# Performance work log

Measured on AMD Instinct MI355X. Metric: run time of the kernel, lower is better.

Reference implementation:

```python
import jax, jax.numpy as jnp
import numpy as np

NUM_EXPERTS = 64
TOP_K = 2
TEMPERATURE = 1.0
MOMENTUM = 0.9


def _l2norm(x, axis=-1):
    # torch F.normalize: x / max(||x||, eps)
    n = jnp.linalg.norm(x, axis=axis, keepdims=True)
    return x / jnp.maximum(n, 1e-12)


def setup_inputs() -> dict:
    key = jax.random.key(0)
    k1, k2 = jax.random.split(key)
    hidden_states = jax.random.normal(k1, (4, 4096, 2048), dtype=jnp.float32)
    centers = _l2norm(jax.random.normal(k2, (NUM_EXPERTS, 2048), dtype=jnp.float32))
    return {"hidden_states": hidden_states, "centers": centers}


def reference(hidden_states, centers):
    B, T, H = hidden_states.shape
    flat = hidden_states.reshape(-1, H).astype(jnp.float32)  # [N, H]
    N = flat.shape[0]

    # cosine-similarity logits
    reps_n = _l2norm(flat)
    centers_n = _l2norm(centers)
    temp = jnp.maximum(jnp.float32(TEMPERATURE), 1e-6)
    logits = (reps_n @ centers_n.T) / temp  # [N, E]

    probs = jax.nn.softmax(logits, axis=-1)
    top_w, top_ids = jax.lax.top_k(probs, TOP_K)  # [N, k]
    top_w = top_w / (jnp.sum(top_w, axis=-1, keepdims=True) + 1e-9)

    # EMA center update from top-1 routed expert (training+update path)
    route = top_ids[:, 0]  # [N]
    sums = jax.ops.segment_sum(flat, route, num_segments=NUM_EXPERTS)  # [E, H]
    counts = jax.ops.segment_sum(jnp.ones((N, 1), jnp.float32), route,
                                 num_segments=NUM_EXPERTS)  # [E, 1]
    means = sums / (counts + 1e-6)
    updated = _l2norm(MOMENTUM * centers + (1.0 - MOMENTUM) * means)
    new_centers = jnp.where(counts > 0, updated, centers)

    top_ids = top_ids.reshape(B, T, TOP_K)
    top_w = top_w.reshape(B, T, TOP_K)
    return top_ids, top_w, new_centers
```

## Files before the change

### kernel.cpp

```cpp
#include <hip/hip_runtime.h>
#include <math.h>

#define NTOK 16384
#define HDIM 2048
#define NEXP 64
#define KK   32
#define TAU  5e-5f
#define MAXB 2048
#define KP2  40
#define LTS2 68

typedef __attribute__((ext_vector_type(8))) short short8;
typedef __attribute__((ext_vector_type(4))) float f32x4;
typedef __attribute__((ext_vector_type(2))) unsigned int uint2v;


__global__ __launch_bounds__(256)
void zero_kernel(float* p, int n) {
  int i = blockIdx.x * 256 + threadIdx.x;
  if (i < n) p[i] = 0.0f;
}

__device__ __forceinline__ float block_reduce_sum(float v, float* red) {
  #pragma unroll
  for (int o = 32; o > 0; o >>= 1) v += __shfl_down(v, o, 64);
  int lane = threadIdx.x & 63;
  int wid  = threadIdx.x >> 6;
  if (lane == 0) red[wid] = v;
  __syncthreads();
  float s = red[0] + red[1] + red[2] + red[3];
  __syncthreads();
  return s;
}

__device__ __forceinline__ double block_reduce_sum_f64(double v, double* red) {
  const int tid = threadIdx.x;
  red[tid] = v;
  __syncthreads();
  if (tid < 128) red[tid] += red[tid + 128];
  __syncthreads();
  if (tid < 64)  red[tid] += red[tid + 64];
  __syncthreads();
  double s = 0.0;
  if (tid < 64) {
    s = red[tid];
    #pragma unroll
    for (int o = 32; o > 0; o >>= 1) s += __shfl_down(s, o, 64);
  }
  if (tid == 0) red[0] = s;
  __syncthreads();
  s = red[0];
  __syncthreads();
  return s;
}

__global__ __launch_bounds__(256)
void cnorm_kernel(const float* __restrict__ c, float* __restrict__ inv_nc) {
  __shared__ float red[4];
  int e = blockIdx.x;
  float ss = 0.f;
  #pragma unroll
  for (int j = 0; j < 8; ++j) {
    float v = c[e * HDIM + threadIdx.x + j * 256];
    ss += v * v;
  }
  float tot = block_reduce_sum(ss, red);
  if (threadIdx.x == 0) inv_nc[e] = 1.0f / fmaxf(sqrtf(tot), 1e-12f);
}

__global__ __launch_bounds__(256)
void cprep_kernel(const float* __restrict__ c, float* __restrict__ inv_nc,
                  float* __restrict__ bn, unsigned short* __restrict__ cbh,
                  unsigned short* __restrict__ cbl, int* __restrict__ zr,
                  int* __restrict__ cnt) {
  __shared__ float red[4];
  __shared__ double redd[256];
  __shared__ float s_nc;
  const int e = blockIdx.x;
  const int tid = threadIdx.x;
  if (e == 0 && tid < 128) zr[tid] = 0;
  if (e == 1 && tid < 64)  cnt[tid] = 0;
  const float* cr = c + (size_t)e * HDIM;
  float ss = 0.f;
  double acc = 0.0;
  #pragma unroll
  for (int j = 0; j < 8; ++j) {
    float v = cr[tid + j * 256];
    ss += v * v;
    double dv = (double)v;
    acc += dv * dv;
  }
  float tot = block_reduce_sum(ss, red);
  double cn = block_reduce_sum_f64(acc, redd);
  if (tid == 0) {
    inv_nc[e] = 1.0f / fmaxf(sqrtf(tot), 1e-12f);
    s_nc = (float)fmax(sqrt(cn), 1e-12);
  }
  __syncthreads();
  const double nc = (double)s_nc;
  #pragma unroll
  for (int j = 0; j < 8; ++j) {
    const int k = tid + j * 256;
    const float v = cr[k];
    bn[(size_t)e * HDIM + k] = (float)((double)v / nc);
    unsigned u = __float_as_uint(v);
    unsigned h = u & 0xffff0000u;
    float r = v - __uint_as_float(h);
    cbh[(size_t)e * HDIM + k] = (unsigned short)(u >> 16);
    cbl[(size_t)e * HDIM + k] = (unsigned short)(__float_as_uint(r) >> 16);
  }
}

__device__ __forceinline__ void cvt2(float v0, float v1, unsigned &hi, unsigned &lo) {
  unsigned u0 = __float_as_uint(v0);
  unsigned u1 = __float_as_uint(v1);
  unsigned h0 = u0 & 0xffff0000u;
  unsigned h1 = u1 & 0xffff0000u;
  float r0 = v0 - __uint_as_float(h0);
  float r1 = v1 - __uint_as_float(h1);
  hi = (u0 >> 16) | h1;
  lo = (__float_as_uint(r0) >> 16) | (__float_as_uint(r1) & 0xffff0000u);
}

__global__ __launch_bounds__(256)
void gemm_part(const float* __restrict__ x,
               const unsigned short* __restrict__ cbh,
               const unsigned short* __restrict__ cbl,
               float* __restrict__ lp, float* __restrict__ xnp) {
  __shared__ __align__(16) unsigned short smem[10240];
  unsigned short (*Ah)[KP2] = (unsigned short (*)[KP2])(smem);
  unsigned short (*Al)[KP2] = (unsigned short (*)[KP2])(smem + 2560);
  unsigned short (*Bh)[KP2] = (unsigned short (*)[KP2])(smem + 5120);
  unsigned short (*Bl)[KP2] = (unsigned short (*)[KP2])(smem + 7680);

  const int tid  = threadIdx.x;
  const int mt   = blockIdx.x >> 3;
  const int ks   = blockIdx.x & 7;
  const int t0   = mt * 64;
  const int kb   = ks * 256;
  const int sr   = tid >> 2;
  const int sq   = (tid & 3) * 8;
  const int lane = tid & 63;
  const int w    = tid >> 6;
  const int tw   = (w & 1) * 32;
  const int ew   = (w >> 1) * 32;
  const int fr   = lane & 15;
  const int fk   = (lane >> 4) * 8;

  const float*          xrow  = x   + (size_t)(t0 + sr) * HDIM + kb + sq;
  const unsigned short* bhrow = cbh + (size_t)sr * HDIM + kb + sq;
  const unsigned short* blrow = cbl + (size_t)sr * HDIM + kb + sq;

  f32x4 xp0, xp1;
  short8 bhp, blp;
  float nacc = 0.f;

  xp0 = *(const f32x4*)(xrow);
  xp1 = *(const f32x4*)(xrow + 4);
  bhp = *(const short8*)(bhrow);
  blp = *(const short8*)(blrow);

  f32x4 acc[2][2];
  #pragma unroll
  for (int mi = 0; mi < 2; ++mi)
    #pragma unroll
    for (int ni = 0; ni < 2; ++ni)
      acc[mi][ni] = (f32x4){0.f, 0.f, 0.f, 0.f};

  for (int it = 0; it < 8; ++it) {
    __syncthreads();
    {
      unsigned h01, l01, h23, l23, h45, l45, h67, l67;
      cvt2(xp0.x, xp0.y, h01, l01);
      cvt2(xp0.z, xp0.w, h23, l23);
      cvt2(xp1.x, xp1.y, h45, l45);
      cvt2(xp1.z, xp1.w, h67, l67);
      *(uint2v*)&Ah[sr][sq]     = (uint2v){h01, h23};
      *(uint2v*)&Ah[sr][sq + 4] = (uint2v){h45, h67};
      *(uint2v*)&Al[sr][sq]     = (uint2v){l01, l23};
      *(uint2v*)&Al[sr][sq + 4] = (uint2v){l45, l67};
      nacc += xp0.x*xp0.x + xp0.y*xp0.y + xp0.z*xp0.z + xp0.w*xp0.w
            + xp1.x*xp1.x + xp1.y*xp1.y + xp1.z*xp1.z + xp1.w*xp1.w;
      *(short8*)&Bh[sr][sq] = bhp;
      *(short8*)&Bl[sr][sq] = blp;
    }
    __syncthreads();
    if (it < 7) {
      const int o = (it + 1) * KK;
      xp0 = *(const f32x4*)(xrow + o);
      xp1 = *(const f32x4*)(xrow + o + 4);
      bhp = *(const short8*)(bhrow + o);
      blp = *(const short8*)(blrow + o);
    }
    short8 ah0 = *(const short8*)&Ah[tw + fr][fk];
    short8 ah1 = *(const short8*)&Ah[tw + 16 + fr][fk];
    short8 al0 = *(const short8*)&Al[tw + fr][fk];
    short8 al1 = *(const short8*)&Al[tw + 16 + fr][fk];
    #pragma unroll
    for (int ni = 0; ni < 2; ++ni) {
      short8 bh = *(const short8*)&Bh[ew + ni * 16 + fr][fk];
      short8 bl = *(const short8*)&Bl[ew + ni * 16 + fr][fk];
      acc[0][ni] = __builtin_amdgcn_mfma_f32_16x16x32_bf16(ah0, bh, acc[0][ni], 0, 0, 0);
      acc[0][ni] = __builtin_amdgcn_mfma_f32_16x16x32_bf16(ah0, bl, acc[0][ni], 0, 0, 0);
      acc[0][ni] = __builtin_amdgcn_mfma_f32_16x16x32_bf16(al0, bh, acc[0][ni], 0, 0, 0);
      acc[1][ni] = __builtin_amdgcn_mfma_f32_16x16x32_bf16(ah1, bh, acc[1][ni], 0, 0, 0);
      acc[1][ni] = __builtin_amdgcn_mfma_f32_16x16x32_bf16(ah1, bl, acc[1][ni], 0, 0, 0);
      acc[1][ni] = __builtin_amdgcn_mfma_f32_16x16x32_bf16(al1, bh, acc[1][ni], 0, 0, 0);
    }
  }

  float s = nacc;
  s += __shfl_xor(s, 1, 64);
  s += __shfl_xor(s, 2, 64);
  if ((tid & 3) == 0) xnp[ks * NTOK + t0 + sr] = s;

  __syncthreads();
  float* lt = (float*)smem;
  const int tloc = tw + (lane >> 4) * 4;
  #pragma unroll
  for (int mi = 0; mi < 2; ++mi)
    #pragma unroll
    for (int ni = 0; ni < 2; ++ni)
      *(f32x4*)&lt[(ew + ni * 16 + fr) * LTS2 + tloc + mi * 16] = acc[mi][ni];
  __syncthreads();
  #pragma unroll
  for (int n = 0; n < 16; ++n) {
    const int f = tid + n * 256;
    const int e = f >> 6;
    const int t = f & 63;
    lp[(size_t)(ks * NEXP + e) * NTOK + t0 + t] = lt[e * LTS2 + t];
  }
}

__global__ __launch_bounds__(512)
void softmax2_kernel(const float* __restrict__ lp, const float* __restrict__ xnp,
                     const float* __restrict__ inv_nc, float* __restrict__ out,
                     int* __restrict__ route, int* __restrict__ nflag,
                     int* __restrict__ flags, int* __restrict__ cursor,
                     int* __restrict__ cnt, int* __restrict__ bucket,
                     int* __restrict__ posa) {
  __shared__ float lg[NEXP][68];
  __shared__ float snc[NEXP];
  const int tid  = threadIdx.x;
  const int lane = tid & 63;
  const int w    = tid >> 6;
  const int kg   = w >> 2;
  const int eg   = (w & 3) * 16;
  const int t0   = blockIdx.x * 64;
  const int t    = t0 + lane;
  if (tid < NEXP) snc[tid] = inv_nc[tid];

  float p[16];
  const float* base = lp + (size_t)(kg * 4 * NEXP + eg) * NTOK + t;
  #pragma unroll
  for (int e = 0; e < 16; ++e) {
    const float* q = base + (size_t)e * NTOK;
    float a0 = q[0];
    float a1 = q[(size_t)NEXP * NTOK];
    float a2 = q[(size_t)2 * NEXP * NTOK];
    float a3 = q[(size_t)3 * NEXP * NTOK];
    p[e] = (a0 + a1) + (a2 + a3);
  }
  if (kg == 0) {
    #pragma unroll
    for (int e = 0; e < 16; ++e) lg[eg + e][lane] = p[e];
  }
  __syncthreads();
  if (kg == 1) {
    #pragma unroll
    for (int e = 0; e < 16; ++e) lg[eg + e][lane] += p[e];
  }
  __syncthreads();

  if (tid < 64) {
    float xs2 = 0.f;
    #pragma unroll
    for (int k = 0; k < 8; ++k) xs2 += xnp[k * NTOK + t];
    const float inv_nx = 1.0f / fmaxf(sqrtf(xs2), 1e-12f);
    float m1 = -1e30f, m2 = -1e30f, m3 = -1e30f;
    int i1 = 0, i2 = 0;
    #pragma unroll
    for (int e = 0; e < NEXP; ++e) {
      float l = lg[e][lane] * snc[e] * inv_nx;
      if (l > m1)      { m3 = m2; m2 = m1; i2 = i1; m1 = l; i1 = e; }
      else if (l > m2) { m3 = m2; m2 = l; i2 = e; }
      else if (l > m3) { m3 = l; }
    }
    float Z = 0.f;
    #pragma unroll
    for (int e = 0; e < NEXP; ++e)
      Z += expf(lg[e][lane] * snc[e] * inv_nx - m1);
    const float p1w = 1.0f / Z;
    const float p2w = expf(m2 - m1) / Z;
    const float s2  = p1w + p2w + 1e-9f;
    out[t * 2 + 0] = (float)i1;
    out[t * 2 + 1] = (float)i2;
    out[2 * NTOK + t * 2 + 0] = p1w / s2;
    out[2 * NTOK + t * 2 + 1] = p2w / s2;
    route[t] = i1;
    const int p0 = atomicAdd(&cursor[i1], 1);
    atomicAdd(&cnt[i1], 1);
    if (p0 < MAXB) bucket[i1 * MAXB + p0] = t;
    posa[t] = p0;
    if ((m1 - m2) < TAU || (m2 - m3) < TAU) {
      int idx = atomicAdd(nflag, 1);
      flags[idx] = t;
    }
  }
}

__global__ __launch_bounds__(256)
void refine_np_kernel(const float* __restrict__ x, const float* __restrict__ bn,
                      float* __restrict__ out, int* __restrict__ route,
                      const int* __restrict__ nflag, const int* __restrict__ flags,
                      int* __restrict__ cursor, int* __restrict__ cnt,
                      int* __restrict__ bucket, int* __restrict__ posa) {
  __shared__ float a_lds[HDIM];
  __shared__ double redd[256];
  __shared__ float lf[NEXP];
  __shared__ float s_nx;
  const int tid  = threadIdx.x;
  const int lane = tid & 63;
  const int w    = tid >> 6;
  const int n = *nflag;
  for (int j = blockIdx.x; j < n; j += gridDim.x) {
    const int t = flags[j];
    const float* xr = x + (size_t)t * HDIM;
    double xacc = 0.0;
    #pragma unroll
    for (int i = 0; i < 8; ++i) {
      double v = (double)xr[tid + 256 * i];
      xacc += v * v;
    }
    double xn = block_reduce_sum_f64(xacc, redd);
    if (tid == 0) s_nx = (float)fmax(sqrt(xn), 1e-12);
    __syncthreads();
    const double nx = (double)s_nx;
    #pragma unroll
    for (int i = 0; i < 8; ++i) {
      int k = tid + 256 * i;
      a_lds[k] = (float)((double)xr[k] / nx);
    }
    __syncthreads();
    #pragma unroll 1
    for (int ei = 0; ei < 16; ++ei) {
      const int e = w * 16 + ei;
      const float* br = bn + (size_t)e * HDIM;
      double d = 0.0;
      #pragma unroll 8
      for (int i = 0; i < 32; ++i) {
        int k = lane + 64 * i;
        d += (double)a_lds[k] * (double)br[k];
      }
      #pragma unroll
      for (int o = 32; o > 0; o >>= 1) d += __shfl_down(d, o, 64);
      if (lane == 0) lf[e] = (float)d;
    }
    __syncthreads();
    if (tid == 0) {
      float m32 = lf[0];
      for (int ee = 1; ee < NEXP; ++ee) m32 = fmaxf(m32, lf[ee]);
      float ex[NEXP];
      for (int ee = 0; ee < NEXP; ++ee)
        ex[ee] = (float)exp((double)(lf[ee] - m32));
      float r[8];
      #pragma unroll
      for (int q = 0; q < 8; ++q) r[q] = ex[q];
      for (int i = 8; i < NEXP; i += 8)
        #pragma unroll
        for (int q = 0; q < 8; ++q) r[q] += ex[i + q];
      const float Z = ((r[0] + r[1]) + (r[2] + r[3])) + ((r[4] + r[5]) + (r[6] + r[7]));
      float p1 = -1.f, p2 = -1.f;
      int i1 = 0, i2 = 0;
      for (int ee = 0; ee < NEXP; ++ee) {
        float p = ex[ee] / Z;
        if (p > p1)      { p2 = p1; i2 = i1; p1 = p; i1 = ee; }
        else if (p > p2) { p2 = p; i2 = ee; }
      }
      const float s = (p1 + p2) + 1e-9f;
      out[t * 2 + 0] = (float)i1;
      out[t * 2 + 1] = (float)i2;
      out[2 * NTOK + t * 2 + 0] = p1 / s;
      out[2 * NTOK + t * 2 + 1] = p2 / s;
      const int old = route[t];
      if (i1 != old) {
        const int p_old = posa[t];
        if (p_old < MAXB) bucket[old * MAXB + p_old] = -1;
        atomicSub(&cnt[old], 1);
        const int p = atomicAdd(&cursor[i1], 1);
        atomicAdd(&cnt[i1], 1);
        if (p < MAXB) bucket[i1 * MAXB + p] = t;
        posa[t] = p;
        route[t] = i1;
      }
    }
    __syncthreads();
  }
}

__global__ __launch_bounds__(64)
void refine_np_slow(const float* __restrict__ x, const float* __restrict__ c,
                    float* __restrict__ out, int* __restrict__ route,
                    const int* __restrict__ nflag, const int* __restrict__ flags) {
  __shared__ float lf[NEXP];
  const int e = threadIdx.x;
  const int n = *nflag;
  for (int j = blockIdx.x; j < n; j += gridDim.x) {
    const int t = flags[j];
    const float* xr = x + (size_t)t * HDIM;
    const float* cr = c + (size_t)e * HDIM;
    double xn = 0.0, cn = 0.0;
    for (int k = 0; k < HDIM; ++k) {
      double xv = (double)xr[k];
      double cv = (double)cr[k];
      xn += xv * xv;
      cn += cv * cv;
    }
    const float nx32 = (float)fmax(sqrt(xn), 1e-12);
    const float nc32 = (float)fmax(sqrt(cn), 1e-12);
    double d = 0.0;
    for (int k = 0; k < HDIM; ++k) {
      float a = (float)((double)xr[k] / (double)nx32);
      float b = (float)((double)cr[k] / (double)nc32);
      d += (double)a * (double)b;
    }
    lf[e] = (float)d;
    __syncthreads();
    if (e == 0) {
      float m32 = lf[0];
      for (int ee = 1; ee < NEXP; ++ee) m32 = fmaxf(m32, lf[ee]);
      float ex[NEXP];
      for (int ee = 0; ee < NEXP; ++ee)
        ex[ee] = (float)exp((double)(lf[ee] - m32));
      float r[8];
      #pragma unroll
      for (int q = 0; q < 8; ++q) r[q] = ex[q];
      for (int i = 8; i < NEXP; i += 8)
        #pragma unroll
        for (int q = 0; q < 8; ++q) r[q] += ex[i + q];
      const float Z = ((r[0] + r[1]) + (r[2] + r[3])) + ((r[4] + r[5]) + (r[6] + r[7]));
      float p1 = -1.f, p2 = -1.f;
      int i1 = 0, i2 = 0;
      for (int ee = 0; ee < NEXP; ++ee) {
        float p = ex[ee] / Z;
        if (p > p1)      { p2 = p1; i2 = i1; p1 = p; i1 = ee; }
        else if (p > p2) { p2 = p; i2 = ee; }
      }
      const float s = (p1 + p2) + 1e-9f;
      out[t * 2 + 0] = (float)i1;
      out[t * 2 + 1] = (float)i2;
      out[2 * NTOK + t * 2 + 0] = p1 / s;
      out[2 * NTOK + t * 2 + 1] = p2 / s;
      route[t] = i1;
    }
    __syncthreads();
  }
}

__global__ __launch_bounds__(256)
void segsum_part(const float* __restrict__ x, const int* __restrict__ cursor,
                 const int* __restrict__ bucket, float* __restrict__ psum) {
  __shared__ f32x4 part[4][64];
  const int e   = blockIdx.x >> 5;
  const int hc  = (blockIdx.x >> 2) & 7;
  const int ts  = blockIdx.x & 3;
  const int hb  = hc * 256;
  const int tid = threadIdx.x;
  const int rg  = tid >> 6;
  const int cc  = tid & 63;
  int n = cursor[e];
  if (n > MAXB) n = MAXB;
  const int nq = (n + 3) >> 2;
  const int lo = ts * nq;
  const int hi = min(lo + nq, n);
  const int* bk = bucket + e * MAXB;
  f32x4 a = (f32x4){0.f, 0.f, 0.f, 0.f};
  #pragma unroll 4
  for (int i = lo + rg; i < hi; i += 4) {
    const int r = bk[i];
    if (r >= 0) a += *(const f32x4*)(x + (size_t)r * HDIM + hb + cc * 4);
  }
  part[rg][cc] = a;
  __syncthreads();
  if (tid < 64) {
    f32x4 s = part[0][tid] + part[1][tid] + part[2][tid] + part[3][tid];
    *(f32x4*)&psum[(size_t)(ts * NEXP + e) * HDIM + hb + tid * 4] = s;
  }
}

__global__ __launch_bounds__(256)
void finalize4_kernel(const float* __restrict__ c, const float* __restrict__ psum,
                      const int* __restrict__ counts, float* __restrict__ out) {
  __shared__ float red[4];
  const int e = blockIdx.x;
  const int tid = threadIdx.x;
  const float cnt = (float)counts[e];
  const float minv = 1.0f / (cnt + 1e-6f);
  float u[8], cv[8];
  float ss = 0.f;
  #pragma unroll
  for (int j = 0; j < 8; ++j) {
    int h = tid + j * 256;
    cv[j] = c[e * HDIM + h];
    float sm = psum[(size_t)(0 * NEXP + e) * HDIM + h]
             + psum[(size_t)(1 * NEXP + e) * HDIM + h]
             + psum[(size_t)(2 * NEXP + e) * HDIM + h]
             + psum[(size_t)(3 * NEXP + e) * HDIM + h];
    float mean = sm * minv;
    u[j] = 0.9f * cv[j] + 0.1f * mean;
    ss += u[j] * u[j];
  }
  float tot = block_reduce_sum(ss, red);
  float sc = 1.0f / fmaxf(sqrtf(tot), 1e-12f);
  const bool nz = cnt > 0.f;
  #pragma unroll
  for (int j = 0; j < 8; ++j) {
    int h = tid + j * 256;
    out[4 * NTOK + e * HDIM + h] = nz ? u[j] * sc : cv[j];
  }
}

__global__ __launch_bounds__(256)
void finalize_kernel(const float* __restrict__ c, const float* __restrict__ sums,
                     const int* __restrict__ counts, float* __restrict__ out) {
  __shared__ float red[4];
  const int e = blockIdx.x;
  const int tid = threadIdx.x;
  const float cnt = (float)counts[e];
  const float minv = 1.0f / (cnt + 1e-6f);
  float u[8], cv[8];
  float ss = 0.f;
  #pragma unroll
  for (int j = 0; j < 8; ++j) {
    int h = tid + j * 256;
    cv[j] = c[e * HDIM + h];
    float mean = sums[e * HDIM + h] * minv;
    u[j] = 0.9f * cv[j] + 0.1f * mean;
    ss += u[j] * u[j];
  }
  float tot = block_reduce_sum(ss, red);
  float sc = 1.0f / fmaxf(sqrtf(tot), 1e-12f);
  const bool nz = cnt > 0.f;
  #pragma unroll
  for (int j = 0; j < 8; ++j) {
    int h = tid + j * 256;
    out[4 * NTOK + e * HDIM + h] = nz ? u[j] * sc : cv[j];
  }
}

__global__ __launch_bounds__(256)
void router_kernel(const float* __restrict__ x, const float* __restrict__ c,
                   const float* __restrict__ inv_nc, float* __restrict__ out,
                   int* __restrict__ route, int* __restrict__ nflag,
                   int* __restrict__ flags) {
  __shared__ __align__(16) float xs[64][36];
  __shared__ float lgs[64][67];
  const int tid  = threadIdx.x;
  const int lane = tid & 63;
  const int w    = tid >> 6;
  const int t0   = blockIdx.x * 64;
  const int e0   = __builtin_amdgcn_readfirstlane(w * 16);
  const float* cb = c + (size_t)e0 * HDIM;
  const int st = tid >> 3;
  const int sk = (tid & 7) * 4;
  float acc[16];
  #pragma unroll
  for (int e = 0; e < 16; ++e) acc[e] = 0.f;
  float nacc = 0.f;
  float4 p0 = *(const float4*)&x[(size_t)(t0 + st)      * HDIM + sk];
  float4 p1 = *(const float4*)&x[(size_t)(t0 + st + 32) * HDIM + sk];
  for (int k0 = 0; k0 < HDIM; k0 += 32) {
    __syncthreads();
    *(float4*)&xs[st][sk]      = p0;
    *(float4*)&xs[st + 32][sk] = p1;
    __syncthreads();
    const int kn = k0 + 32;
    if (kn < HDIM) {
      p0 = *(const float4*)&x[(size_t)(t0 + st)      * HDIM + kn + sk];
      p1 = *(const float4*)&x[(size_t)(t0 + st + 32) * HDIM + kn + sk];
    }
    float a[32];
    #pragma unroll
    for (int j = 0; j < 32; j += 4) {
      float4 v = *(const float4*)&xs[lane][j];
      a[j] = v.x; a[j+1] = v.y; a[j+2] = v.z; a[j+3] = v.w;
    }
    if (w == 0) {
      #pragma unroll
      for (int j = 0; j < 32; ++j) nacc += a[j] * a[j];
    }
    #pragma unroll
    for (int e = 0; e < 16; ++e) {
      const float* br = cb + (size_t)e * HDIM + k0;
      #pragma unroll
      for (int j = 0; j < 32; j += 4) {
        float4 bv = *(const float4*)&br[j];
        acc[e] += a[j]*bv.x + a[j+1]*bv.y + a[j+2]*bv.z + a[j+3]*bv.w;
      }
    }
  }
  #pragma unroll
  for (int e = 0; e < 16; ++e) lgs[lane][e0 + e] = acc[e] * inv_nc[e0 + e];
  __syncthreads();
  if (w == 0) {
    const float inv_nx = 1.0f / fmaxf(sqrtf(nacc), 1e-12f);
    float m1 = -1e30f, m2 = -1e30f, m3 = -1e30f;
    int i1 = 0, i2 = 0;
    for (int e = 0; e < NEXP; ++e) {
      float l = lgs[lane][e] * inv_nx;
      if (l > m1)      { m3 = m2; m2 = m1; i2 = i1; m1 = l; i1 = e; }
      else if (l > m2) { m3 = m2; m2 = l; i2 = e; }
      else if (l > m3) { m3 = l; }
    }
    float Z = 0.f;
    for (int e = 0; e < NEXP; ++e) Z += expf(lgs[lane][e] * inv_nx - m1);
    const float p1w = 1.0f / Z;
    const float p2w = expf(m2 - m1) / Z;
    const float s   = p1w + p2w + 1e-9f;
    const int tg = t0 + lane;
    out[tg * 2 + 0] = (float)i1;
    out[tg * 2 + 1] = (float)i2;
    out[2 * NTOK + tg * 2 + 0] = p1w / s;
    out[2 * NTOK + tg * 2 + 1] = p2w / s;
    route[tg] = i1;
    if ((m1 - m2) < TAU || (m2 - m3) < TAU) {
      int idx = atomicAdd(nflag, 1);
      flags[idx] = tg;
    }
  }
}

__global__ __launch_bounds__(512)
void segsum_kernel(const float* __restrict__ x, const int* __restrict__ route,
                   float* __restrict__ sums, int* __restrict__ counts) {
  __shared__ float ls[NEXP * 256];
  __shared__ int lcnt[NEXP];
  const int tid  = threadIdx.x;
  const int lane = tid & 63;
  const int w    = tid >> 6;
  const int hc   = blockIdx.x & 7;
  const int tg   = blockIdx.x >> 3;
  const int hb   = hc * 256;
  #pragma unroll
  for (int i = 0; i < 32; ++i) ls[tid + i * 512] = 0.f;
  if (tid < NEXP) lcnt[tid] = 0;
  __syncthreads();
  const int tbase = tg * 512 + w * 64;
  #pragma unroll 4
  for (int i = 0; i < 64; ++i) {
    const int t = tbase + i;
    const int e = route[t];
    const float* xr = x + (size_t)t * HDIM + hb + lane;
    #pragma unroll
    for (int j = 0; j < 4; ++j)
      atomicAdd(&ls[e * 256 + lane + 64 * j], xr[64 * j]);
    if (hc == 0 && lane == 0) atomicAdd(&lcnt[e], 1);
  }
  __syncthreads();
  #pragma unroll
  for (int i = tid; i < NEXP * 256; i += 512) {
    const int e = i >> 8, h = i & 255;
    atomicAdd(&sums[e * HDIM + hb + h], ls[i]);
  }
  if (hc == 0 && tid < NEXP && lcnt[tid] > 0) atomicAdd(&counts[tid], lcnt[tid]);
}

extern "C" void kernel_launch(void* const* d_in, const int* in_sizes, int n_in,
                              void* d_out, int out_size, void* d_ws, size_t ws_size,
                              hipStream_t stream) {
  const float* x = (const float*)d_in[0];
  const float* c = (const float*)d_in[1];
  float* out = (float*)d_out;
  float* ws = (float*)d_ws;

  float* inv_nc = ws;
  int*   cursor = (int*)(ws + 64);
  int*   nflag  = (int*)(ws + 128);
  int*   route  = (int*)(ws + 192);
  int*   flags  = (int*)(ws + 16576);
  float* sums   = ws + 32960;
  float* bn     = ws + 164032;
  unsigned short* cbh = (unsigned short*)(ws + 295104);
  unsigned short* cbl = (unsigned short*)(ws + 360640);
  int*   bucket = (int*)(ws + 426176);
  float* psum   = ws + 557248;
  int*   posa   = (int*)(ws + 1081536);
  int*   cnt    = (int*)(ws + 1097920);
  float* lp     = ws + 1097984;
  float* xnp    = ws + 9486592;

  const size_t NEED = 9617664ull * 4ull;
  if (ws_size >= NEED) {
    cprep_kernel<<<NEXP, 256, 0, stream>>>(c, inv_nc, bn, cbh, cbl, cursor, cnt);
    gemm_part<<<2048, 256, 0, stream>>>(x, cbh, cbl, lp, xnp);
    softmax2_kernel<<<NTOK / 64, 512, 0, stream>>>(lp, xnp, inv_nc, out, route,
                                                   nflag, flags, cursor, cnt, bucket, posa);
    refine_np_kernel<<<512, 256, 0, stream>>>(x, bn, out, route, nflag, flags,
                                              cursor, cnt, bucket, posa);
    segsum_part<<<2048, 256, 0, stream>>>(x, cursor, bucket, psum);
    finalize4_kernel<<<NEXP, 256, 0, stream>>>(c, psum, cnt, out);
  } else {
    zero_kernel<<<1, 256, 0, stream>>>(ws + 64, 128);
    zero_kernel<<<512, 256, 0, stream>>>(sums, 131072);
    cnorm_kernel<<<NEXP, 256, 0, stream>>>(c, inv_nc);
    router_kernel<<<NTOK / 64, 256, 0, stream>>>(x, c, inv_nc, out, route, nflag, flags);
    refine_np_slow<<<1024, 64, 0, stream>>>(x, c, out, route, nflag, flags);
    segsum_kernel<<<256, 512, 0, stream>>>(x, route, sums, cursor);
    finalize_kernel<<<NEXP, 256, 0, stream>>>(c, sums, cursor, out);
  }
}
```

Before: 312.2 us.

## Double-buffer GEMM register prefetch and parallelize softmax top-k across wave lanes

The logits GEMM kernel now prefetches global tiles into two alternating register sets, so the load for step it+2 is issued while step it is computed. The softmax kernel stops using 64 threads for the whole top-2 and softmax work. Each wave now handles 8 tokens, with one expert per lane, and finds top-3 values and the softmax denominator by cross-lane shuffle reductions. This spreads the serial 64-expert scan over all 512 threads, at the cost of many shuffles per token. It also changes the LDS padding, which may cause bank conflicts on the transposed lg reads.

```diff
diff --git a/kernel.cpp b/kernel.cpp
--- a/kernel.cpp
+++ b/kernel.cpp
@@ -151,14 +151,9 @@
   const unsigned short* bhrow = cbh + (size_t)sr * HDIM + kb + sq;
   const unsigned short* blrow = cbl + (size_t)sr * HDIM + kb + sq;
 
-  f32x4 xp0, xp1;
-  short8 bhp, blp;
   float nacc = 0.f;
-
-  xp0 = *(const f32x4*)(xrow);
-  xp1 = *(const f32x4*)(xrow + 4);
-  bhp = *(const short8*)(bhrow);
-  blp = *(const short8*)(blrow);
+  f32x4 Ax0, Ax1, Bx0, Bx1;
+  short8 Abh, Abl, Bbh, Bbl;
 
   f32x4 acc[2][2];
   #pragma unroll
@@ -167,47 +162,63 @@
     for (int ni = 0; ni < 2; ++ni)
       acc[mi][ni] = (f32x4){0.f, 0.f, 0.f, 0.f};
 
-  for (int it = 0; it < 8; ++it) {
-    __syncthreads();
-    {
-      unsigned h01, l01, h23, l23, h45, l45, h67, l67;
-      cvt2(xp0.x, xp0.y, h01, l01);
-      cvt2(xp0.z, xp0.w, h23, l23);
-      cvt2(xp1.x, xp1.y, h45, l45);
-      cvt2(xp1.z, xp1.w, h67, l67);
-      *(uint2v*)&Ah[sr][sq]     = (uint2v){h01, h23};
-      *(uint2v*)&Ah[sr][sq + 4] = (uint2v){h45, h67};
-      *(uint2v*)&Al[sr][sq]     = (uint2v){l01, l23};
-      *(uint2v*)&Al[sr][sq + 4] = (uint2v){l45, l67};
-      nacc += xp0.x*xp0.x + xp0.y*xp0.y + xp0.z*xp0.z + xp0.w*xp0.w
-            + xp1.x*xp1.x + xp1.y*xp1.y + xp1.z*xp1.z + xp1.w*xp1.w;
-      *(short8*)&Bh[sr][sq] = bhp;
-      *(short8*)&Bl[sr][sq] = blp;
-    }
-    __syncthreads();
-    if (it < 7) {
-      const int o = (it + 1) * KK;
-      xp0 = *(const f32x4*)(xrow + o);
-      xp1 = *(const f32x4*)(xrow + o + 4);
-      bhp = *(const short8*)(bhrow + o);
-      blp = *(const short8*)(blrow + o);
-    }
-    short8 ah0 = *(const short8*)&Ah[tw + fr][fk];
-    short8 ah1 = *(const short8*)&Ah[tw + 16 + fr][fk];
-    short8 al0 = *(const short8*)&Al[tw + fr][fk];
-    short8 al1 = *(const short8*)&Al[tw + 16 + fr][fk];
-    #pragma unroll
-    for (int ni = 0; ni < 2; ++ni) {
-      short8 bh = *(const short8*)&Bh[ew + ni * 16 + fr][fk];
-      short8 bl = *(const short8*)&Bl[ew + ni * 16 + fr][fk];
-      acc[0][ni] = __builtin_amdgcn_mfma_f32_16x16x32_bf16(ah0, bh, acc[0][ni], 0, 0, 0);
-      acc[0][ni] = __builtin_amdgcn_mfma_f32_16x16x32_bf16(ah0, bl, acc[0][ni], 0, 0, 0);
-      acc[0][ni] = __builtin_amdgcn_mfma_f32_16x16x32_bf16(al0, bh, acc[0][ni], 0, 0, 0);
-      acc[1][ni] = __builtin_amdgcn_mfma_f32_16x16x32_bf16(ah1, bh, acc[1][ni], 0, 0, 0);
-      acc[1][ni] = __builtin_amdgcn_mfma_f32_16x16x32_bf16(ah1, bl, acc[1][ni], 0, 0, 0);
-      acc[1][ni] = __builtin_amdgcn_mfma_f32_16x16x32_bf16(al1, bh, acc[1][ni], 0, 0, 0);
-    }
-  }
+  #define LDREG(P, it_) do { const int o_ = (it_) * KK;                   \
+    P##x0 = *(const f32x4*)(xrow + o_);                                   \
+    P##x1 = *(const f32x4*)(xrow + o_ + 4);                               \
+    P##bh = *(const short8*)(bhrow + o_);                                 \
+    P##bl = *(const short8*)(blrow + o_); } while (0)
+
+  #define STAGE(P) do {                                                   \
+    unsigned h01, l01, h23, l23, h45, l45, h67, l67;                      \
+    cvt2(P##x0.x, P##x0.y, h01, l01);                                     \
+    cvt2(P##x0.z, P##x0.w, h23, l23);                                     \
+    cvt2(P##x1.x, P##x1.y, h45, l45);                                     \
+    cvt2(P##x1.z, P##x1.w, h67, l67);                                     \
+    *(uint2v*)&Ah[sr][sq]     = (uint2v){h01, h23};                       \
+    *(uint2v*)&Ah[sr][sq + 4] = (uint2v){h45, h67};                       \
+    *(uint2v*)&Al[sr][sq]     = (uint2v){l01, l23};                       \
+    *(uint2v*)&Al[sr][sq + 4] = (uint2v){l45, l67};                       \
+    nacc += P##x0.x*P##x0.x + P##x0.y*P##x0.y + P##x0.z*P##x0.z + P##x0.w*P##x0.w \
+          + P##x1.x*P##x1.x + P##x1.y*P##x1.y + P##x1.z*P##x1.z + P##x1.w*P##x1.w; \
+    *(short8*)&Bh[sr][sq] = P##bh;                                        \
+    *(short8*)&Bl[sr][sq] = P##bl; } while (0)
+
+  #define MFMAS() do {                                                    \
+    short8 ah0 = *(const short8*)&Ah[tw + fr][fk];                        \
+    short8 ah1 = *(const short8*)&Ah[tw + 16 + fr][fk];                   \
+    short8 al0 = *(const short8*)&Al[tw + fr][fk];                        \
+    short8 al1 = *(const short8*)&Al[tw + 16 + fr][fk];                   \
+    _Pragma("unroll")                                                     \
+    for (int ni = 0; ni < 2; ++ni) {                                      \
+      short8 bh = *(const short8*)&Bh[ew + ni * 16 + fr][fk];             \
+      short8 bl = *(const short8*)&Bl[ew + ni * 16 + fr][fk];             \
+      acc[0][ni] = __builtin_amdgcn_mfma_f32_16x16x32_bf16(ah0, bh, acc[0][ni], 0, 0, 0); \
+      acc[0][ni] = __builtin_amdgcn_mfma_f32_16x16x32_bf16(ah0, bl, acc[0][ni], 0, 0, 0); \
+      acc[0][ni] = __builtin_amdgcn_mfma_f32_16x16x32_bf16(al0, bh, acc[0][ni], 0, 0, 0); \
+      acc[1][ni] = __builtin_amdgcn_mfma_f32_16x16x32_bf16(ah1, bh, acc[1][ni], 0, 0, 0); \
+      acc[1][ni] = __builtin_amdgcn_mfma_f32_16x16x32_bf16(ah1, bl, acc[1][ni], 0, 0, 0); \
+      acc[1][ni] = __builtin_amdgcn_mfma_f32_16x16x32_bf16(al1, bh, acc[1][ni], 0, 0, 0); \
+    } } while (0)
+
+  LDREG(A, 0);
+  LDREG(B, 1);
+
+  #pragma unroll 1
+  for (int it = 0; it < 8; it += 2) {
+    __syncthreads();
+    STAGE(A);
+    __syncthreads();
+    if (it + 2 < 8) LDREG(A, it + 2);
+    MFMAS();
+    __syncthreads();
+    STAGE(B);
+    __syncthreads();
+    if (it + 3 < 8) LDREG(B, it + 3);
+    MFMAS();
+  }
+  #undef LDREG
+  #undef STAGE
+  #undef MFMAS
 
   float s = nacc;
   s += __shfl_xor(s, 1, 64);
@@ -239,7 +250,8 @@
                      int* __restrict__ flags, int* __restrict__ cursor,
                      int* __restrict__ cnt, int* __restrict__ bucket,
                      int* __restrict__ posa) {
-  __shared__ float lg[NEXP][68];
+  __shared__ float lg[NEXP][65];
+  __shared__ float xn_s[64];
   __shared__ float snc[NEXP];
   const int tid  = threadIdx.x;
   const int lane = tid & 63;
@@ -247,64 +259,86 @@
   const int kg   = w >> 2;
   const int eg   = (w & 3) * 16;
   const int t0   = blockIdx.x * 64;
-  const int t    = t0 + lane;
   if (tid < NEXP) snc[tid] = inv_nc[tid];
 
   float p[16];
-  const float* base = lp + (size_t)(kg * 4 * NEXP + eg) * NTOK + t;
-  #pragma unroll
-  for (int e = 0; e < 16; ++e) {
-    const float* q = base + (size_t)e * NTOK;
-    float a0 = q[0];
-    float a1 = q[(size_t)NEXP * NTOK];
-    float a2 = q[(size_t)2 * NEXP * NTOK];
-    float a3 = q[(size_t)3 * NEXP * NTOK];
-    p[e] = (a0 + a1) + (a2 + a3);
-  }
-  if (kg == 0) {
-    #pragma unroll
-    for (int e = 0; e < 16; ++e) lg[eg + e][lane] = p[e];
+  {
+    const int t = t0 + lane;
+    const float* base = lp + (size_t)(kg * 4 * NEXP + eg) * NTOK + t;
+    #pragma unroll
+    for (int e = 0; e < 16; ++e) {
+      const float* q = base + (size_t)e * NTOK;
+      float a0 = q[0];
+      float a1 = q[(size_t)NEXP * NTOK];
+      float a2 = q[(size_t)2 * NEXP * NTOK];
+      float a3 = q[(size_t)3 * NEXP * NTOK];
+      p[e] = (a0 + a1) + (a2 + a3);
+    }
+    if (kg == 0) {
+      #pragma unroll
+      for (int e = 0; e < 16; ++e) lg[eg + e][lane] = p[e];
+    }
   }
   __syncthreads();
   if (kg == 1) {
     #pragma unroll
     for (int e = 0; e < 16; ++e) lg[eg + e][lane] += p[e];
   }
-  __syncthreads();
-
   if (tid < 64) {
     float xs2 = 0.f;
     #pragma unroll
-    for (int k = 0; k < 8; ++k) xs2 += xnp[k * NTOK + t];
-    const float inv_nx = 1.0f / fmaxf(sqrtf(xs2), 1e-12f);
-    float m1 = -1e30f, m2 = -1e30f, m3 = -1e30f;
-    int i1 = 0, i2 = 0;
-    #pragma unroll
-    for (int e = 0; e < NEXP; ++e) {
-      float l = lg[e][lane] * snc[e] * inv_nx;
-      if (l > m1)      { m3 = m2; m2 = m1; i2 = i1; m1 = l; i1 = e; }
-      else if (l > m2) { m3 = m2; m2 = l; i2 = e; }
-      else if (l > m3) { m3 = l; }
-    }
-    float Z = 0.f;
-    #pragma unroll
-    for (int e = 0; e < NEXP; ++e)
-      Z += expf(lg[e][lane] * snc[e] * inv_nx - m1);
-    const float p1w = 1.0f / Z;
-    const float p2w = expf(m2 - m1) / Z;
-    const float s2  = p1w + p2w + 1e-9f;
-    out[t * 2 + 0] = (float)i1;
-    out[t * 2 + 1] = (float)i2;
-    out[2 * NTOK + t * 2 + 0] = p1w / s2;
-    out[2 * NTOK + t * 2 + 1] = p2w / s2;
-    route[t] = i1;
-    const int p0 = atomicAdd(&cursor[i1], 1);
-    atomicAdd(&cnt[i1], 1);
-    if (p0 < MAXB) bucket[i1 * MAXB + p0] = t;
-    posa[t] = p0;
-    if ((m1 - m2) < TAU || (m2 - m3) < TAU) {
-      int idx = atomicAdd(nflag, 1);
-      flags[idx] = t;
+    for (int k = 0; k < 8; ++k) xs2 += xnp[k * NTOK + t0 + tid];
+    xn_s[tid] = xs2;
+  }
+  __syncthreads();
+
+  #pragma unroll 1
+  for (int j = 0; j < 8; ++j) {
+    const int tl = w * 8 + j;
+    const int t  = t0 + tl;
+    const float inv_nx = 1.0f / fmaxf(sqrtf(xn_s[tl]), 1e-12f);
+    const float l = lg[lane][tl] * snc[lane] * inv_nx;
+    float v = l; int idx = lane;
+    #pragma unroll
+    for (int o = 32; o > 0; o >>= 1) {
+      float ov = __shfl_xor(v, o, 64);
+      int   oi = __shfl_xor(idx, o, 64);
+      if (ov > v || (ov == v && oi < idx)) { v = ov; idx = oi; }
+    }
+    const float m1 = v; const int i1 = idx;
+    v = (lane == i1) ? -1e30f : l; idx = lane;
+    #pragma unroll
+    for (int o = 32; o > 0; o >>= 1) {
+      float ov = __shfl_xor(v, o, 64);
+      int   oi = __shfl_xor(idx, o, 64);
+      if (ov > v || (ov == v && oi < idx)) { v = ov; idx = oi; }
+    }
+    const float m2 = v; const int i2 = idx;
+    v = (lane == i1 || lane == i2) ? -1e30f : l;
+    #pragma unroll
+    for (int o = 32; o > 0; o >>= 1) v = fmaxf(v, __shfl_xor(v, o, 64));
+    const float m3 = v;
+    float ze = expf(l - m1);
+    #pragma unroll
+    for (int o = 32; o > 0; o >>= 1) ze += __shfl_xor(ze, o, 64);
+    if (lane == 0) {
+      const float Z   = ze;
+      const float p1w = 1.0f / Z;
+      const float p2w = expf(m2 - m1) / Z;
+      const float s2  = p1w + p2w + 1e-9f;
+      out[t * 2 + 0] = (float)i1;
+      out[t * 2 + 1] = (float)i2;
+      out[2 * NTOK + t * 2 + 0] = p1w / s2;
+      out[2 * NTOK + t * 2 + 1] = p2w / s2;
+      route[t] = i1;
+      const int p0 = atomicAdd(&cursor[i1], 1);
+      atomicAdd(&cnt[i1], 1);
+      if (p0 < MAXB) bucket[i1 * MAXB + p0] = t;
+      posa[t] = p0;
+      if ((m1 - m2) < TAU || (m2 - m3) < TAU) {
+        int fidx = atomicAdd(nflag, 1);
+        flags[fidx] = t;
+      }
     }
   }
 }
```

Result: slower. 353.4 us (+13.2%).
